# Optimization experiments

Hardware: AMD Instinct MI355X
Metric: run time of the kernel (lower is better)

Reference implementation:

```python
import jax, jax.numpy as jnp
import numpy as np

BATCH, SEQ, FEAT, LAYERS = 32, 512, 1024, 2


def setup_inputs() -> dict:
    key = jax.random.key(0)
    ks = jax.random.split(key, 1 + 3 * LAYERS)
    inp = {"x": jax.random.normal(ks[0], (BATCH, SEQ, FEAT), dtype=jnp.float32)}
    scale_i = 1.0 / np.sqrt(FEAT)
    for l in range(LAYERS):
        # flax OptimizedLSTMCell: input dense (no bias) + hidden dense (with bias),
        # both producing 4*features (gates i, f, g, o concatenated).
        inp[f"Wi{l}"] = jax.random.normal(ks[1 + 3 * l], (FEAT, 4 * FEAT), dtype=jnp.float32) * scale_i
        inp[f"Wh{l}"] = jax.random.normal(ks[2 + 3 * l], (FEAT, 4 * FEAT), dtype=jnp.float32) * scale_i
        inp[f"b{l}"] = jnp.zeros((4 * FEAT,), dtype=jnp.float32)
    return inp


def _lstm_layer(x, Wi, Wh, b):
    # x: [B, T, F_in]; returns [B, T, F]
    B = x.shape[0]
    F = Wh.shape[0]
    # Precompute input projections for all steps (one big GEMM): [B, T, 4F]
    xz = jnp.einsum("btf,fg->btg", x, Wi) + b

    def step(carry, xz_t):
        c, h = carry
        z = xz_t + h @ Wh  # [B, 4F]
        i, f, g, o = jnp.split(z, 4, axis=-1)
        c_new = jax.nn.sigmoid(f) * c + jax.nn.sigmoid(i) * jnp.tanh(g)
        h_new = jax.nn.sigmoid(o) * jnp.tanh(c_new)
        return (c_new, h_new), h_new

    init = (jnp.zeros((B, F), x.dtype), jnp.zeros((B, F), x.dtype))
    _, ys = jax.lax.scan(step, init, jnp.swapaxes(xz, 0, 1))  # scan over time
    return jnp.swapaxes(ys, 0, 1)


def reference(x, Wi0, Wh0, b0, Wi1, Wh1, b1):
    y = _lstm_layer(x, Wi0, Wh0, b0)
    y = _lstm_layer(y, Wi1, Wh1, b1)
    return y
```

## Files before the change

### kernel.cpp

```cpp
#include <hip/hip_runtime.h>
#include <hip/hip_bf16.h>
#include <hip/hip_fp16.h>


typedef _Float16 f16x8 __attribute__((ext_vector_type(8)));
typedef __fp16 fp16x2 __attribute__((ext_vector_type(2)));
typedef float f32x4 __attribute__((ext_vector_type(4)));

#define NB 32
#define NTT 512
#define NF 1024
#define NG 4096
#define TFE (NTT * NF)
#define NWG 256
#define NTHR 512

#define W_F16X8 8192
#define W_BYTES (W_F16X8 * 16)
#define ZQSEG 33
#define Z_FLOATS (8 * 16 * ZQSEG)
#define LDS_BYTES (W_BYTES + Z_FLOATS * 4)
#define RINGB 65536
#define MBOX 4096

__device__ __forceinline__ float sigm(float v) { return 1.0f / (1.0f + __expf(-v)); }
__device__ __forceinline__ float tanh_s(float v) {
  float a = fabsf(v);
  float e = __expf(-2.0f * a);
  float t = (1.0f - e) / (1.0f + e);
  return v < 0.0f ? -t : t;
}

__device__ __forceinline__ unsigned pk(float a, float b) {
  union { fp16x2 h2; unsigned u; } c;
  c.h2 = __builtin_amdgcn_cvt_pkrtz(a, b);
  return c.u;
}

__device__ __forceinline__ f16x8 cvt8(f32x4 lo, f32x4 hi) {
  union { unsigned u[4]; f16x8 h8; } u;
  u.u[0] = pk(lo[0], lo[1]);
  u.u[1] = pk(lo[2], lo[3]);
  u.u[2] = pk(hi[0], hi[1]);
  u.u[3] = pk(hi[2], hi[3]);
  return u.h8;
}

__device__ __forceinline__ unsigned ldu(const unsigned* p) {
  unsigned v;
  asm volatile("global_load_dword %0, %1, off sc0 sc1\n\ts_waitcnt vmcnt(0)"
               : "=&v"(v) : "v"(p) : "memory");
  return v;
}

__device__ __forceinline__ void ld4(f16x8 o[4], const char* p) {
  asm volatile("global_load_dwordx4 %0, %4, off sc0 sc1\n\t"
               "global_load_dwordx4 %1, %4, off offset:64 sc0 sc1\n\t"
               "global_load_dwordx4 %2, %4, off offset:128 sc0 sc1\n\t"
               "global_load_dwordx4 %3, %4, off offset:192 sc0 sc1"
               : "=&v"(o[0]), "=&v"(o[1]), "=&v"(o[2]), "=&v"(o[3])
               : "v"(p) : "memory");
}

__global__ __launch_bounds__(NTHR, 1) void lstm_persist(
    const float* __restrict__ x,
    const float* __restrict__ Wi0, const float* __restrict__ Wh0, const float* __restrict__ bv0,
    const float* __restrict__ Wi1, const float* __restrict__ Wh1, const float* __restrict__ bv1,
    float* __restrict__ out, unsigned short* __restrict__ hring_u16,
    unsigned* __restrict__ bar) {
  extern __shared__ char lds[];
  f16x8* Wl = (f16x8*)lds;
  float* Zr = (float*)(lds + W_BYTES);

  const int wg = blockIdx.x;
  const int tid = threadIdx.x;
  const int role = wg >> 7;
  const int fg = wg & 127;
  const int fbase = fg * 8;
  const int w = tid >> 6;
  const int Kq = w >> 1;
  const int mt = w & 1;
  const int lane = tid & 63;
  const int lr = lane & 15;
  const int g = lane >> 4;
  unsigned gen = 0;

  auto gridbar = [&]() {
    asm volatile("s_waitcnt vmcnt(0) lgkmcnt(0)" ::: "memory");
    __syncthreads();
    ++gen;
    if (tid == 0)
      asm volatile("global_store_dword %0, %1, off sc0 sc1"
                   :: "v"(&bar[wg * 16]), "v"(gen) : "memory");
    if (wg == 0) {
      if (tid < 64) {
        const unsigned* f0 = &bar[(tid * 4 + 0) * 16];
        const unsigned* f1 = &bar[(tid * 4 + 1) * 16];
        const unsigned* f2 = &bar[(tid * 4 + 2) * 16];
        const unsigned* f3 = &bar[(tid * 4 + 3) * 16];
        for (;;) {
          unsigned v0, v1, v2, v3;
          asm volatile("global_load_dword %0, %4, off sc0 sc1\n\t"
                       "global_load_dword %1, %5, off sc0 sc1\n\t"
                       "global_load_dword %2, %6, off sc0 sc1\n\t"
                       "global_load_dword %3, %7, off sc0 sc1\n\t"
                       "s_waitcnt vmcnt(0)"
                       : "=&v"(v0), "=&v"(v1), "=&v"(v2), "=&v"(v3)
                       : "v"(f0), "v"(f1), "v"(f2), "v"(f3)
                       : "memory");
          if (__all((v0 >= gen) & (v1 >= gen) & (v2 >= gen) & (v3 >= gen))) break;
        }
      }
      __syncthreads();
      if (tid < 256)
        asm volatile("global_store_dword %0, %1, off sc0 sc1"
                     :: "v"(&bar[MBOX + tid * 16]), "v"(gen) : "memory");
      __syncthreads();
    } else {
      if (tid == 0) {
        const unsigned* mb = &bar[MBOX + wg * 16];
        while (ldu(mb) < gen) __builtin_amdgcn_s_sleep(1);
      }
      __syncthreads();
    }
  };

  const float* Wi = role ? Wi1 : Wi0;
  const float* Wh = role ? Wh1 : Wh0;
  const float* bv = role ? bv1 : bv0;
  unsigned* h0 = (unsigned*)hring_u16;
  unsigned* h1 = (unsigned*)(hring_u16 + 2 * NB * NF);
  unsigned* hmine = role ? h1 : h0;

  for (int idx = tid; idx < 16384; idx += NTHR) {
    const int k = idx >> 3, chunk = idx & 7;
    const int q = chunk >> 1, half = chunk & 1;
    const float* src = (k < NF) ? (Wi + (size_t)k * NG) : (Wh + (size_t)(k - NF) * NG);
    const f32x4 v = *(const f32x4*)(src + q * NF + fbase + half * 4);
    const int s = k >> 5, kg = (k >> 3) & 3, jj = k & 7;
#pragma unroll
    for (int j = 0; j < 4; ++j) {
      const int c = q * 8 + half * 4 + j;
      _Float16* dst = (_Float16*)&Wl[((s * 2 + (c >> 4)) * 64) + kg * 16 + (c & 15)];
      dst[jj] = (_Float16)v[j];
    }
  }
  if (tid < 128) {
    const int b = tid >> 2, fp = tid & 3;
    __hip_atomic_store(&hmine[b * 512 + (fbase >> 1) + fp], 0u,
                       __ATOMIC_RELAXED, __HIP_MEMORY_SCOPE_AGENT);
  }
  float bias[4][2];
  if (tid < 128) {
    const int fp = tid & 3;
#pragma unroll
    for (int q = 0; q < 4; ++q) {
      bias[q][0] = bv[q * NF + fbase + 2 * fp];
      bias[q][1] = bv[q * NF + fbase + 2 * fp + 1];
    }
  }
  float cst[2] = {0.f, 0.f};
  __syncthreads();
  gridbar();

  for (int rd = 0; rd <= NTT; ++rd) {
    const bool doit = role == 0 ? (rd < NTT) : (rd >= 1);
    const int t = role == 0 ? rd : rd - 1;

    if (doit) {
      f32x4 acc0 = {0.f, 0.f, 0.f, 0.f}, acc1 = {0.f, 0.f, 0.f, 0.f};
      const int brow = mt * 16 + lr;

      bool f16src;
      const char* hp = nullptr;
      const float* xp = nullptr;
      if (role == 0) {
        if (Kq < 2) {
          xp = x + (size_t)brow * TFE + (size_t)t * NF + Kq * 512 + g * 8;
          f16src = false;
        } else {
          hp = (const char*)h0 + (size_t)(rd & 1) * RINGB + brow * 2048
               + ((Kq - 2) * 512 + g * 8) * 2;
          f16src = true;
        }
      } else {
        if (Kq < 2)
          hp = (const char*)h0 + (size_t)(rd & 1) * RINGB + brow * 2048
               + (Kq * 512 + g * 8) * 2;
        else
          hp = (const char*)h1 + (size_t)((rd - 1) & 1) * RINGB + brow * 2048
               + ((Kq - 2) * 512 + g * 8) * 2;
        f16src = true;
      }

      if (f16src) {
        f16x8 T0[4], T1[4], T2[4], T3[4];
        ld4(T0, hp); ld4(T1, hp + 256);
        asm volatile("s_waitcnt vmcnt(4)" ::: "memory");
        __builtin_amdgcn_sched_barrier(0);
        ld4(T2, hp + 512);
#pragma unroll
        for (int kk = 0; kk < 4; ++kk) {
          const int s = Kq * 16 + kk;
          acc0 = __builtin_amdgcn_mfma_f32_16x16x32_f16(T0[kk], Wl[(s * 2 + 0) * 64 + lane], acc0, 0, 0, 0);
          acc1 = __builtin_amdgcn_mfma_f32_16x16x32_f16(T0[kk], Wl[(s * 2 + 1) * 64 + lane], acc1, 0, 0, 0);
        }
        asm volatile("s_waitcnt vmcnt(4)" ::: "memory");
        __builtin_amdgcn_sched_barrier(0);
        ld4(T3, hp + 768);
#pragma unroll
        for (int kk = 0; kk < 4; ++kk) {
          const int s = Kq * 16 + 4 + kk;
          acc0 = __builtin_amdgcn_mfma_f32_16x16x32_f16(T1[kk], Wl[(s * 2 + 0) * 64 + lane], acc0, 0, 0, 0);
          acc1 = __builtin_amdgcn_mfma_f32_16x16x32_f16(T1[kk], Wl[(s * 2 + 1) * 64 + lane], acc1, 0, 0, 0);
        }
        asm volatile("s_waitcnt vmcnt(4)" ::: "memory");
        __builtin_amdgcn_sched_barrier(0);
#pragma unroll
        for (int kk = 0; kk < 4; ++kk) {
          const int s = Kq * 16 + 8 + kk;
          acc0 = __builtin_amdgcn_mfma_f32_16x16x32_f16(T2[kk], Wl[(s * 2 + 0) * 64 + lane], acc0, 0, 0, 0);
          acc1 = __builtin_amdgcn_mfma_f32_16x16x32_f16(T2[kk], Wl[(s * 2 + 1) * 64 + lane], acc1, 0, 0, 0);
        }
        asm volatile("s_waitcnt vmcnt(0)" ::: "memory");
        __builtin_amdgcn_sched_barrier(0);
#pragma unroll
        for (int kk = 0; kk < 4; ++kk) {
          const int s = Kq * 16 + 12 + kk;
          acc0 = __builtin_amdgcn_mfma_f32_16x16x32_f16(T3[kk], Wl[(s * 2 + 0) * 64 + lane], acc0, 0, 0, 0);
          acc1 = __builtin_amdgcn_mfma_f32_16x16x32_f16(T3[kk], Wl[(s * 2 + 1) * 64 + lane], acc1, 0, 0, 0);
        }
      } else {
#pragma unroll
        for (int ks = 0; ks < 16; ++ks) {
          const int s = Kq * 16 + ks;
          const f32x4 al = *(const f32x4*)(xp + ks * 32);
          const f32x4 ah = *(const f32x4*)(xp + ks * 32 + 4);
          const f16x8 A = cvt8(al, ah);
          acc0 = __builtin_amdgcn_mfma_f32_16x16x32_f16(A, Wl[(s * 2 + 0) * 64 + lane], acc0, 0, 0, 0);
          acc1 = __builtin_amdgcn_mfma_f32_16x16x32_f16(A, Wl[(s * 2 + 1) * 64 + lane], acc1, 0, 0, 0);
        }
      }

      {
        float* zb = Zr + (size_t)w * 16 * ZQSEG;
#pragma unroll
        for (int reg = 0; reg < 4; ++reg) {
          zb[(g * 4 + reg) * ZQSEG + lr] = acc0[reg];
          zb[(g * 4 + reg) * ZQSEG + 16 + lr] = acc1[reg];
        }
      }
      __syncthreads();

      if (tid < 128) {
        const int b = tid >> 2, fp = tid & 3;
        const int bmt = b >> 4, row = b & 15;
        float hv[2];
#pragma unroll
        for (int e = 0; e < 2; ++e) {
          const int f = 2 * fp + e;
          float zq[4];
#pragma unroll
          for (int q = 0; q < 4; ++q) {
            const int c = q * 8 + f;
            float sum = bias[q][e];
#pragma unroll
            for (int kq = 0; kq < 4; ++kq)
              sum += Zr[((kq * 2 + bmt) * 16 + row) * ZQSEG + c];
            zq[q] = sum;
          }
          const float cn = sigm(zq[1]) * cst[e] + sigm(zq[0]) * tanh_s(zq[2]);
          hv[e] = sigm(zq[3]) * tanh_s(cn);
          cst[e] = cn;
        }
        const int wph = role == 0 ? ((rd + 1) & 1) : (rd & 1);
        __hip_atomic_store(&hmine[wph * NB * 512 + b * 512 + (fbase >> 1) + fp],
                           pk(hv[0], hv[1]), __ATOMIC_RELAXED, __HIP_MEMORY_SCOPE_AGENT);
        if (role == 1)
          *(float2*)(out + (size_t)b * TFE + (size_t)t * NF + fbase + 2 * fp) =
              make_float2(hv[0], hv[1]);
      }
    }
    gridbar();
  }
}

extern "C" void kernel_launch(void* const* d_in, const int* in_sizes, int n_in,
                              void* d_out, int out_size, void* d_ws, size_t ws_size,
                              hipStream_t stream) {
  (void)in_sizes; (void)n_in; (void)out_size; (void)ws_size;
  const float* x   = (const float*)d_in[0];
  const float* Wi0 = (const float*)d_in[1];
  const float* Wh0 = (const float*)d_in[2];
  const float* b0  = (const float*)d_in[3];
  const float* Wi1 = (const float*)d_in[4];
  const float* Wh1 = (const float*)d_in[5];
  const float* b1  = (const float*)d_in[6];
  float* out = (float*)d_out;

  unsigned short* hring = (unsigned short*)d_ws;
  unsigned* bar = (unsigned*)((char*)d_ws + 262144);

  (void)hipMemsetAsync(bar, 0, 32768, stream);

  (void)hipFuncSetAttribute((const void*)lstm_persist,
                            hipFuncAttributeMaxDynamicSharedMemorySize, LDS_BYTES);

  lstm_persist<<<dim3(NWG), dim3(NTHR), LDS_BYTES, stream>>>(
      x, Wi0, Wh0, b0, Wi1, Wh1, b1, out, hring, bar);
}
```

Before: 4.239 ms.

## Split grid barrier into arrive/wait so input-projection waves skip the wait

The grid barrier becomes two parts: a non-blocking arrive at the end of each step and a mailbox wait. Only waves that need the previous hidden state call the wait, and they call it just before loading it. In layer-0 workgroups, the waves that multiply by x start each step without waiting, so their MFMA work overlaps the barrier latency. All four h loads are now issued up front with staged waitcnts. The cost is that every h-consuming wave polls the mailbox instead of a single thread, which adds memory traffic and can slightly delay release.

```diff
diff --git a/kernel.cpp b/kernel.cpp
--- a/kernel.cpp
+++ b/kernel.cpp
@@ -85,7 +85,7 @@
   const int g = lane >> 4;
   unsigned gen = 0;
 
-  auto gridbar = [&]() {
+  auto arrive = [&]() {
     asm volatile("s_waitcnt vmcnt(0) lgkmcnt(0)" ::: "memory");
     __syncthreads();
     ++gen;
@@ -116,12 +116,14 @@
         asm volatile("global_store_dword %0, %1, off sc0 sc1"
                      :: "v"(&bar[MBOX + tid * 16]), "v"(gen) : "memory");
       __syncthreads();
-    } else {
-      if (tid == 0) {
-        const unsigned* mb = &bar[MBOX + wg * 16];
-        while (ldu(mb) < gen) __builtin_amdgcn_s_sleep(1);
-      }
-      __syncthreads();
+    }
+  };
+
+  auto waitgen = [&]() {
+    const unsigned* mb = &bar[MBOX + wg * 16];
+    for (;;) {
+      if (ldu(mb) >= gen) break;
+      __builtin_amdgcn_s_sleep(1);
     }
   };
 
@@ -161,7 +163,8 @@
   }
   float cst[2] = {0.f, 0.f};
   __syncthreads();
-  gridbar();
+  arrive();
+  waitgen();
 
   for (int rd = 0; rd <= NTT; ++rd) {
     const bool doit = role == 0 ? (rd < NTT) : (rd >= 1);
@@ -171,66 +174,8 @@
       f32x4 acc0 = {0.f, 0.f, 0.f, 0.f}, acc1 = {0.f, 0.f, 0.f, 0.f};
       const int brow = mt * 16 + lr;
 
-      bool f16src;
-      const char* hp = nullptr;
-      const float* xp = nullptr;
-      if (role == 0) {
-        if (Kq < 2) {
-          xp = x + (size_t)brow * TFE + (size_t)t * NF + Kq * 512 + g * 8;
-          f16src = false;
-        } else {
-          hp = (const char*)h0 + (size_t)(rd & 1) * RINGB + brow * 2048
-               + ((Kq - 2) * 512 + g * 8) * 2;
-          f16src = true;
-        }
-      } else {
-        if (Kq < 2)
-          hp = (const char*)h0 + (size_t)(rd & 1) * RINGB + brow * 2048
-               + (Kq * 512 + g * 8) * 2;
-        else
-          hp = (const char*)h1 + (size_t)((rd - 1) & 1) * RINGB + brow * 2048
-               + ((Kq - 2) * 512 + g * 8) * 2;
-        f16src = true;
-      }
-
-      if (f16src) {
-        f16x8 T0[4], T1[4], T2[4], T3[4];
-        ld4(T0, hp); ld4(T1, hp + 256);
-        asm volatile("s_waitcnt vmcnt(4)" ::: "memory");
-        __builtin_amdgcn_sched_barrier(0);
-        ld4(T2, hp + 512);
-#pragma unroll
-        for (int kk = 0; kk < 4; ++kk) {
-          const int s = Kq * 16 + kk;
-          acc0 = __builtin_amdgcn_mfma_f32_16x16x32_f16(T0[kk], Wl[(s * 2 + 0) * 64 + lane], acc0, 0, 0, 0);
-          acc1 = __builtin_amdgcn_mfma_f32_16x16x32_f16(T0[kk], Wl[(s * 2 + 1) * 64 + lane], acc1, 0, 0, 0);
-        }
-        asm volatile("s_waitcnt vmcnt(4)" ::: "memory");
-        __builtin_amdgcn_sched_barrier(0);
-        ld4(T3, hp + 768);
-#pragma unroll
-        for (int kk = 0; kk < 4; ++kk) {
-          const int s = Kq * 16 + 4 + kk;
-          acc0 = __builtin_amdgcn_mfma_f32_16x16x32_f16(T1[kk], Wl[(s * 2 + 0) * 64 + lane], acc0, 0, 0, 0);
-          acc1 = __builtin_amdgcn_mfma_f32_16x16x32_f16(T1[kk], Wl[(s * 2 + 1) * 64 + lane], acc1, 0, 0, 0);
-        }
-        asm volatile("s_waitcnt vmcnt(4)" ::: "memory");
-        __builtin_amdgcn_sched_barrier(0);
-#pragma unroll
-        for (int kk = 0; kk < 4; ++kk) {
-          const int s = Kq * 16 + 8 + kk;
-          acc0 = __builtin_amdgcn_mfma_f32_16x16x32_f16(T2[kk], Wl[(s * 2 + 0) * 64 + lane], acc0, 0, 0, 0);
-          acc1 = __builtin_amdgcn_mfma_f32_16x16x32_f16(T2[kk], Wl[(s * 2 + 1) * 64 + lane], acc1, 0, 0, 0);
-        }
-        asm volatile("s_waitcnt vmcnt(0)" ::: "memory");
-        __builtin_amdgcn_sched_barrier(0);
-#pragma unroll
-        for (int kk = 0; kk < 4; ++kk) {
-          const int s = Kq * 16 + 12 + kk;
-          acc0 = __builtin_amdgcn_mfma_f32_16x16x32_f16(T3[kk], Wl[(s * 2 + 0) * 64 + lane], acc0, 0, 0, 0);
-          acc1 = __builtin_amdgcn_mfma_f32_16x16x32_f16(T3[kk], Wl[(s * 2 + 1) * 64 + lane], acc1, 0, 0, 0);
-        }
-      } else {
+      if (role == 0 && w < 4) {
+        const float* xp = x + (size_t)brow * TFE + (size_t)t * NF + Kq * 512 + g * 8;
 #pragma unroll
         for (int ks = 0; ks < 16; ++ks) {
           const int s = Kq * 16 + ks;
@@ -240,6 +185,54 @@
           acc0 = __builtin_amdgcn_mfma_f32_16x16x32_f16(A, Wl[(s * 2 + 0) * 64 + lane], acc0, 0, 0, 0);
           acc1 = __builtin_amdgcn_mfma_f32_16x16x32_f16(A, Wl[(s * 2 + 1) * 64 + lane], acc1, 0, 0, 0);
         }
+      } else {
+        waitgen();
+        const char* hp;
+        if (role == 0)
+          hp = (const char*)h0 + (size_t)(rd & 1) * RINGB + brow * 2048
+               + ((Kq - 2) * 512 + g * 8) * 2;
+        else if (Kq < 2)
+          hp = (const char*)h0 + (size_t)(rd & 1) * RINGB + brow * 2048
+               + (Kq * 512 + g * 8) * 2;
+        else
+          hp = (const char*)h1 + (size_t)((rd + 1) & 1) * RINGB + brow * 2048
+               + ((Kq - 2) * 512 + g * 8) * 2;
+
+        f16x8 T[16];
+        ld4(T + 0, hp);       ld4(T + 4, hp + 256);
+        ld4(T + 8, hp + 512); ld4(T + 12, hp + 768);
+        asm volatile("s_waitcnt vmcnt(12)" ::: "memory");
+        __builtin_amdgcn_sched_barrier(0);
+#pragma unroll
+        for (int kk = 0; kk < 4; ++kk) {
+          const int s = Kq * 16 + kk;
+          acc0 = __builtin_amdgcn_mfma_f32_16x16x32_f16(T[kk], Wl[(s * 2 + 0) * 64 + lane], acc0, 0, 0, 0);
+          acc1 = __builtin_amdgcn_mfma_f32_16x16x32_f16(T[kk], Wl[(s * 2 + 1) * 64 + lane], acc1, 0, 0, 0);
+        }
+        asm volatile("s_waitcnt vmcnt(8)" ::: "memory");
+        __builtin_amdgcn_sched_barrier(0);
+#pragma unroll
+        for (int kk = 0; kk < 4; ++kk) {
+          const int s = Kq * 16 + 4 + kk;
+          acc0 = __builtin_amdgcn_mfma_f32_16x16x32_f16(T[4 + kk], Wl[(s * 2 + 0) * 64 + lane], acc0, 0, 0, 0);
+          acc1 = __builtin_amdgcn_mfma_f32_16x16x32_f16(T[4 + kk], Wl[(s * 2 + 1) * 64 + lane], acc1, 0, 0, 0);
+        }
+        asm volatile("s_waitcnt vmcnt(4)" ::: "memory");
+        __builtin_amdgcn_sched_barrier(0);
+#pragma unroll
+        for (int kk = 0; kk < 4; ++kk) {
+          const int s = Kq * 16 + 8 + kk;
+          acc0 = __builtin_amdgcn_mfma_f32_16x16x32_f16(T[8 + kk], Wl[(s * 2 + 0) * 64 + lane], acc0, 0, 0, 0);
+          acc1 = __builtin_amdgcn_mfma_f32_16x16x32_f16(T[8 + kk], Wl[(s * 2 + 1) * 64 + lane], acc1, 0, 0, 0);
+        }
+        asm volatile("s_waitcnt vmcnt(0)" ::: "memory");
+        __builtin_amdgcn_sched_barrier(0);
+#pragma unroll
+        for (int kk = 0; kk < 4; ++kk) {
+          const int s = Kq * 16 + 12 + kk;
+          acc0 = __builtin_amdgcn_mfma_f32_16x16x32_f16(T[12 + kk], Wl[(s * 2 + 0) * 64 + lane], acc0, 0, 0, 0);
+          acc1 = __builtin_amdgcn_mfma_f32_16x16x32_f16(T[12 + kk], Wl[(s * 2 + 1) * 64 + lane], acc1, 0, 0, 0);
+        }
       }
 
       {
@@ -250,38 +243,38 @@
           zb[(g * 4 + reg) * ZQSEG + 16 + lr] = acc1[reg];
         }
       }
-      __syncthreads();
-
-      if (tid < 128) {
-        const int b = tid >> 2, fp = tid & 3;
-        const int bmt = b >> 4, row = b & 15;
-        float hv[2];
-#pragma unroll
-        for (int e = 0; e < 2; ++e) {
-          const int f = 2 * fp + e;
-          float zq[4];
-#pragma unroll
-          for (int q = 0; q < 4; ++q) {
-            const int c = q * 8 + f;
-            float sum = bias[q][e];
-#pragma unroll
-            for (int kq = 0; kq < 4; ++kq)
-              sum += Zr[((kq * 2 + bmt) * 16 + row) * ZQSEG + c];
-            zq[q] = sum;
-          }
-          const float cn = sigm(zq[1]) * cst[e] + sigm(zq[0]) * tanh_s(zq[2]);
-          hv[e] = sigm(zq[3]) * tanh_s(cn);
-          cst[e] = cn;
-        }
-        const int wph = role == 0 ? ((rd + 1) & 1) : (rd & 1);
-        __hip_atomic_store(&hmine[wph * NB * 512 + b * 512 + (fbase >> 1) + fp],
-                           pk(hv[0], hv[1]), __ATOMIC_RELAXED, __HIP_MEMORY_SCOPE_AGENT);
-        if (role == 1)
-          *(float2*)(out + (size_t)b * TFE + (size_t)t * NF + fbase + 2 * fp) =
-              make_float2(hv[0], hv[1]);
+    }
+    __syncthreads();
+
+    if (doit && tid < 128) {
+      const int b = tid >> 2, fp = tid & 3;
+      const int bmt = b >> 4, row = b & 15;
+      float hv[2];
+#pragma unroll
+      for (int e = 0; e < 2; ++e) {
+        const int f = 2 * fp + e;
+        float zq[4];
+#pragma unroll
+        for (int q = 0; q < 4; ++q) {
+          const int c = q * 8 + f;
+          float sum = bias[q][e];
+#pragma unroll
+          for (int kq = 0; kq < 4; ++kq)
+            sum += Zr[((kq * 2 + bmt) * 16 + row) * ZQSEG + c];
+          zq[q] = sum;
+        }
+        const float cn = sigm(zq[1]) * cst[e] + sigm(zq[0]) * tanh_s(zq[2]);
+        hv[e] = sigm(zq[3]) * tanh_s(cn);
+        cst[e] = cn;
       }
-    }
-    gridbar();
+      const int wph = role == 0 ? ((rd + 1) & 1) : (rd & 1);
+      __hip_atomic_store(&hmine[wph * NB * 512 + b * 512 + (fbase >> 1) + fp],
+                         pk(hv[0], hv[1]), __ATOMIC_RELAXED, __HIP_MEMORY_SCOPE_AGENT);
+      if (role == 1)
+        *(float2*)(out + (size_t)b * TFE + (size_t)t * NF + fbase + 2 * fp) =
+            make_float2(hv[0], hv[1]);
+    }
+    arrive();
   }
 }
 
```

Result: faster. 3.896 ms (-8.1%).
